# Kernel optimization log

Hardware: AMD Instinct MI355X
Metric: run time of the kernel (lower is better)

The kernel has to match this reference:

```python
import jax, jax.numpy as jnp
import numpy as np

TAU = 2.0        # leak time constant
CLAMP = 1000.0   # state clamp in LeakyRNN.recurrence
EPS = 1e-4       # eps in PolicyRNN.evaluate

B, T, H, NI, NA = 64, 2048, 256, 4, 2


def setup_inputs() -> dict:
    key = jax.random.key(0)
    ks = jax.random.split(key, 10)
    state = jax.random.normal(ks[0], (B, T, NI), jnp.float32)
    last_action = jax.random.normal(ks[1], (B, T, NA), jnp.float32)
    reward = jax.random.randint(ks[2], (B, T, NA), 0, 2).astype(jnp.float32)
    hidden_in = jnp.zeros((B, H), jnp.float32)
    W1 = jax.random.normal(ks[3], (H, NI + 2 * NA), jnp.float32) * np.float32(np.sqrt(2.0 / (NI + 2 * NA)))
    b1 = jnp.zeros((H,), jnp.float32)
    Wih = jax.random.normal(ks[4], (H, H), jnp.float32) * np.float32(np.sqrt(2.0 / H))
    Whh_raw = jax.random.normal(ks[5], (H, H), jnp.float32) * np.float32(0.5 / np.sqrt(H))
    W2 = jax.random.normal(ks[6], (H, H), jnp.float32) * np.float32(np.sqrt(2.0 / H))
    b2 = jnp.zeros((H,), jnp.float32)
    W3 = jax.random.normal(ks[7], (NA, H), jnp.float32) * np.float32(np.sqrt(2.0 / H))
    b3 = jnp.zeros((NA,), jnp.float32)
    Qs = jax.random.normal(ks[8], (B, T, NA), jnp.float32)
    # MultLayerAdaptiveSimple with alphas=[1,0]: weight1=[1,0], weight2=[0,1]
    mix_w = jnp.array([[1.0, 0.0], [0.0, 1.0]], jnp.float32)
    return dict(state=state, last_action=last_action, reward=reward,
                hidden_in=hidden_in, W1=W1, b1=b1, Wih=Wih, Whh_raw=Whh_raw,
                W2=W2, b2=b2, W3=W3, b3=b3, Qs=Qs, mix_w=mix_w)


def reference(state, last_action, reward, hidden_in, W1, b1, Wih, Whh_raw,
              W2, b2, W3, b3, Qs, mix_w):
    # (B,T,.) -> (T,B,.) time-major, matching permute(1,0,2)
    x = jnp.concatenate([reward, state, last_action], -1).transpose(1, 0, 2)
    x = jax.nn.relu(x @ W1.T + b1)                     # linear1 + relu

    # IdentityDiagonal parametrization: zero diagonal, subtract I/tau
    Whh = Whh_raw - jnp.diag(jnp.diag(Whh_raw)) - jnp.eye(H, dtype=Whh_raw.dtype) / TAU
    u = x @ Wih.T                                      # precompute input drive (T,B,H)
    leak = 1.0 - 1.0 / TAU

    def step(h, ut):
        h_new = jnp.clip(leak * h + ut + jax.nn.relu(h) @ Whh.T, -CLAMP, CLAMP)
        return h_new, h_new

    hidden_out, ys = jax.lax.scan(step, hidden_in, u)  # ys: (T,B,H)

    y = jax.nn.relu(ys @ W2.T + b2) @ W3.T + b3        # linear2+relu, linear3
    probs = y.transpose(1, 0, 2)                       # (B,T,NA)

    # evaluate() deterministic path with reward-indexed adaptive mixing
    z = (probs == 0.0).astype(probs.dtype) * EPS
    logp = jnp.log(jax.nn.softmax(probs, -1) + z)
    logq = jnp.log(jax.nn.softmax(Qs, -1) + z)
    # SumOne parametrization (p=1) on each MultLayer 2-vector
    w = jnp.clip(mix_w, -1.0, 1.0)
    table = w / jnp.sum(jnp.abs(w), axis=1, keepdims=True)   # (2,2)
    sel = table[reward[:, :, 0].astype(jnp.int32)]           # (B,T,2)
    mixed = logp * sel[..., :1] + logq * sel[..., 1:2]
    return jnp.exp(mixed), hidden_out
```

## Files before the change

kernel.cpp:

```cpp
#include <hip/hip_runtime.h>
#include <hip/hip_bf16.h>
#include <math.h>

#define Bn 64
#define Tn 2048
#define Hn 256

constexpr float LEAK    = 0.5f;
constexpr float NEGDIAG = -0.5f;
constexpr float CLAMP_V = 1000.0f;
constexpr float EPS_V   = 1e-4f;

typedef __attribute__((ext_vector_type(8))) short  short8;
typedef __attribute__((ext_vector_type(4))) float  f32x4;
typedef __attribute__((ext_vector_type(2))) float  f32x2;

#define FAST_BARRIER() do {                                   \
    asm volatile("s_waitcnt lgkmcnt(0)" ::: "memory");        \
    __builtin_amdgcn_s_barrier();                             \
    asm volatile("" ::: "memory");                            \
  } while (0)

__device__ inline short bf16_rne(float x) {
  __hip_bfloat16 h = __float2bfloat16(x);
  return *reinterpret_cast<short*>(&h);
}
__device__ inline float bf16_to_f(short s) {
  union { unsigned u; float f; } c; c.u = ((unsigned)(unsigned short)s) << 16;
  return c.f;
}
__device__ inline unsigned pack2(short a, short b) {
  return (unsigned)(unsigned short)a | ((unsigned)(unsigned short)b << 16);
}
__device__ inline void pkfma(f32x2& a, f32x2 x, f32x2 y) {
  asm("v_pk_fma_f32 %0, %1, %2, %0" : "+v"(a) : "v"(x), "v"(y));
}
#define SWZ(x, imm) __int_as_float(__builtin_amdgcn_ds_swizzle(__float_as_int(x), (imm)))

template <int CTRL>
__device__ __forceinline__ float dpp_recv(float x) {
  return __int_as_float(
      __builtin_amdgcn_update_dpp(0, __float_as_int(x), CTRL, 0xF, 0xF, true));
}

#define SA 40

__global__ __launch_bounds__(512) void g_u(
    const float* __restrict__ reward, const float* __restrict__ state,
    const float* __restrict__ last_action, const float* __restrict__ W1,
    const float* __restrict__ b1, const float* __restrict__ Wih,
    float* __restrict__ u)
{
  __shared__ short Ah[128*SA], Al[128*SA], Bh[256*SA], Bl[256*SA];
  __shared__ __align__(16) float inp_s[128][8];
  __shared__ __align__(16) float w1_s[256][8];
  __shared__ float b1_s[256];
  const int tid = threadIdx.x;
  const int r0  = blockIdx.x * 128;

  for (int idx = tid; idx < 2048; idx += 512) ((float*)w1_s)[idx] = W1[idx];
  if (tid < 256) b1_s[tid] = b1[tid];
  for (int idx = tid; idx < 1024; idx += 512) {
    int rr = idx >> 3, i = idx & 7;
    int r = r0 + rr, b = r & 63, t = r >> 6;
    long base = (long)b * Tn + t;
    float v;
    if (i < 2)      v = reward[base * 2 + i];
    else if (i < 6) v = state[base * 4 + (i - 2)];
    else            v = last_action[base * 2 + (i - 6)];
    inp_s[rr][i] = v;
  }

  const int w    = tid >> 6, lane = tid & 63;
  const int wm   = w >> 2, wn = w & 3;
  const int fr   = lane & 15, fk = lane >> 4;
  f32x4 acc[4][4];
  #pragma unroll
  for (int a = 0; a < 4; ++a)
    #pragma unroll
    for (int c = 0; c < 4; ++c) acc[a][c] = (f32x4){0.f, 0.f, 0.f, 0.f};

  __syncthreads();

  for (int ks = 0; ks < 8; ++ks) {
    const int k0 = ks * 32;
    if (ks) __syncthreads();
    for (int p = tid; p < 2048; p += 512) {
      int rr = p >> 4, kp = (p & 15) * 2;
      int k = k0 + kp;
      float4 iv0 = *reinterpret_cast<const float4*>(&inp_s[rr][0]);
      float4 iv1 = *reinterpret_cast<const float4*>(&inp_s[rr][4]);
      float4 wa0 = *reinterpret_cast<const float4*>(&w1_s[k][0]);
      float4 wa1 = *reinterpret_cast<const float4*>(&w1_s[k][4]);
      float4 wb0 = *reinterpret_cast<const float4*>(&w1_s[k+1][0]);
      float4 wb1 = *reinterpret_cast<const float4*>(&w1_s[k+1][4]);
      float s0 = b1_s[k], s1 = b1_s[k+1];
      s0 = fmaf(iv0.x, wa0.x, s0); s0 = fmaf(iv0.y, wa0.y, s0);
      s0 = fmaf(iv0.z, wa0.z, s0); s0 = fmaf(iv0.w, wa0.w, s0);
      s0 = fmaf(iv1.x, wa1.x, s0); s0 = fmaf(iv1.y, wa1.y, s0);
      s0 = fmaf(iv1.z, wa1.z, s0); s0 = fmaf(iv1.w, wa1.w, s0);
      s1 = fmaf(iv0.x, wb0.x, s1); s1 = fmaf(iv0.y, wb0.y, s1);
      s1 = fmaf(iv0.z, wb0.z, s1); s1 = fmaf(iv0.w, wb0.w, s1);
      s1 = fmaf(iv1.x, wb1.x, s1); s1 = fmaf(iv1.y, wb1.y, s1);
      s1 = fmaf(iv1.z, wb1.z, s1); s1 = fmaf(iv1.w, wb1.w, s1);
      float v0 = fmaxf(s0, 0.f), v1 = fmaxf(s1, 0.f);
      short h0 = bf16_rne(v0), h1 = bf16_rne(v1);
      short l0 = bf16_rne(v0 - bf16_to_f(h0)), l1 = bf16_rne(v1 - bf16_to_f(h1));
      int off = rr * SA + kp;
      *reinterpret_cast<unsigned*>(&Ah[off]) = pack2(h0, h1);
      *reinterpret_cast<unsigned*>(&Al[off]) = pack2(l0, l1);
    }
    for (int c = tid; c < 2048; c += 512) {
      int n = c >> 3, kc = (c & 7) * 4;
      float4 f = *reinterpret_cast<const float4*>(&Wih[n * 256 + k0 + kc]);
      short h0 = bf16_rne(f.x), h1 = bf16_rne(f.y), h2 = bf16_rne(f.z), h3 = bf16_rne(f.w);
      short l0 = bf16_rne(f.x - bf16_to_f(h0)), l1 = bf16_rne(f.y - bf16_to_f(h1));
      short l2 = bf16_rne(f.z - bf16_to_f(h2)), l3 = bf16_rne(f.w - bf16_to_f(h3));
      int off = n * SA + kc;
      *reinterpret_cast<uint2*>(&Bh[off]) = make_uint2(pack2(h0, h1), pack2(h2, h3));
      *reinterpret_cast<uint2*>(&Bl[off]) = make_uint2(pack2(l0, l1), pack2(l2, l3));
    }
    __syncthreads();
    short8 bhf[4], blf[4];
    #pragma unroll
    for (int nf = 0; nf < 4; ++nf) {
      const int brow = wn * 64 + nf * 16 + fr;
      bhf[nf] = *reinterpret_cast<const short8*>(&Bh[brow * SA + fk * 8]);
      blf[nf] = *reinterpret_cast<const short8*>(&Bl[brow * SA + fk * 8]);
    }
    #pragma unroll
    for (int mf = 0; mf < 4; ++mf) {
      const int arow = wm * 64 + mf * 16 + fr;
      short8 ah = *reinterpret_cast<const short8*>(&Ah[arow * SA + fk * 8]);
      short8 al = *reinterpret_cast<const short8*>(&Al[arow * SA + fk * 8]);
      #pragma unroll
      for (int nf = 0; nf < 4; ++nf) {
        acc[mf][nf] = __builtin_amdgcn_mfma_f32_16x16x32_bf16(ah, bhf[nf], acc[mf][nf], 0, 0, 0);
        acc[mf][nf] = __builtin_amdgcn_mfma_f32_16x16x32_bf16(ah, blf[nf], acc[mf][nf], 0, 0, 0);
        acc[mf][nf] = __builtin_amdgcn_mfma_f32_16x16x32_bf16(al, bhf[nf], acc[mf][nf], 0, 0, 0);
      }
    }
  }
  #pragma unroll
  for (int mf = 0; mf < 4; ++mf) {
    const int rbase = r0 + wm * 64 + mf * 16 + (lane >> 4) * 4;
    #pragma unroll
    for (int nf = 0; nf < 4; ++nf) {
      const int n = wn * 64 + nf * 16 + fr;
      #pragma unroll
      for (int j = 0; j < 4; ++j)
        u[(long)(rbase + j) * Hn + n] = acc[mf][nf][j];
    }
  }
}

__global__ __launch_bounds__(512, 2) void k_scan(
    const float* __restrict__ Whh_raw, const float* __restrict__ hidden_in,
    float* __restrict__ ubuf, float* __restrict__ out)
{
  __shared__ __align__(16) float rh[2][256];
  const int tid = threadIdx.x;
  const int w = tid >> 6;
  const int l = tid & 63;
  const int g = (l & 3) | ((l >> 1) & 0x1C);
  const int o = (l >> 2) & 1;
  const int b = blockIdx.x;
  const int key = ((g & 1) << 3) | ((g & 2) << 1) | ((g & 4) >> 1) | ((g & 8) >> 3);

  f32x2 w2[16][4];
  {
    const volatile float* Wv = Whh_raw;
    #pragma unroll
    for (int s = 0; s < 16; ++s) {
      const int j = (w << 5) + (o << 4) + (s ^ key);
      #pragma unroll
      for (int i = 0; i < 4; ++i) {
        const int k = (g << 3) + 2 * i;
        float a = Wv[j * 256 + k];
        float c = Wv[j * 256 + k + 1];
        if (k == j)     a = NEGDIAG;
        if (k + 1 == j) c = NEGDIAG;
        w2[s][i] = (f32x2){a, c};
      }
    }
  }

  const bool owner = (l < 32);
  const int j_own = (w << 5) + (o << 4) + key;

  const int row  = g >> 2;
  const int srot = (((g & 3) << 3) + (row << 2)) & 31;
  const int rd1  = row * 32 + srot;
  const int rd2  = row * 32 + ((srot + 4) & 31);
  const int wrow = j_own >> 5;
  const int wr   = wrow * 32 + (((j_own & 31) + (wrow << 2)) & 31);

  float h = 0.f, u_c = 0.f, u_n = 0.f;
  if (owner) {
    h   = hidden_in[b * Hn + j_own];
    u_c = ubuf[(long)b * Hn + j_own];
    u_n = ubuf[((long)Bn + b) * Hn + j_own];
  }
  const float* u_ptr  = ubuf + ((long)2 * Bn + b) * Hn + j_own;
  float*       ys_ptr = ubuf + (long)b * Hn + j_own;

#define SCAN_STEP(P)                                                         \
  {                                                                          \
    if (owner) rh[P][wr] = fmaxf(h, 0.f);                                    \
    FAST_BARRIER();                                                          \
    float u_pf = 0.f;                                                        \
    if (owner && t + 2 < Tn) u_pf = *u_ptr;                                  \
    const float4 ra = *reinterpret_cast<const float4*>(&rh[P][rd1]);         \
    const float4 rb = *reinterpret_cast<const float4*>(&rh[P][rd2]);         \
    const f32x2 rp0 = {ra.x, ra.y}, rp1 = {ra.z, ra.w};                      \
    const f32x2 rp2 = {rb.x, rb.y}, rp3 = {rb.z, rb.w};                      \
    float v[16];                                                             \
    _Pragma("unroll")                                                        \
    for (int s = 0; s < 16; ++s) {                                           \
      f32x2 c = {0.f, 0.f};                                                  \
      pkfma(c, rp0, w2[s][0]); pkfma(c, rp1, w2[s][1]);                      \
      pkfma(c, rp2, w2[s][2]); pkfma(c, rp3, w2[s][3]);                      \
      v[s] = c.x + c.y;                                                      \
    }                                                                        \
    _Pragma("unroll")                                                        \
    for (int s = 0; s < 8; ++s) v[s] += dpp_recv<0xB1>(v[s + 8]);            \
    _Pragma("unroll")                                                        \
    for (int s = 0; s < 4; ++s) v[s] += dpp_recv<0x4E>(v[s + 4]);            \
    _Pragma("unroll")                                                        \
    for (int s = 0; s < 2; ++s) v[s] += dpp_recv<0x128>(v[s + 2]);           \
    v[0] += SWZ(v[1], 0x401F);                                               \
    {                                                                        \
      float pa = v[0], pb = v[0];                                            \
      asm("v_permlane32_swap_b32 %0, %1" : "+v"(pa), "+v"(pb));              \
      v[0] = pa + pb;                                                        \
    }                                                                        \
    if (owner) {                                                             \
      float hn = fmaf(LEAK, h, u_c) + v[0];                                  \
      hn = fminf(fmaxf(hn, -CLAMP_V), CLAMP_V);                              \
      *ys_ptr = hn;                                                          \
      h = hn; u_c = u_n; u_n = u_pf;                                         \
    }                                                                        \
    ys_ptr += Bn * Hn;                                                       \
    u_ptr  += Bn * Hn;                                                       \
  }

  for (int tt = 0; tt < Tn; tt += 2) {
    { const int t = tt;     SCAN_STEP(0) }
    { const int t = tt + 1; SCAN_STEP(1) }
  }
#undef SCAN_STEP

  if (owner) out[(long)Bn * Tn * 2 + b * Hn + j_own] = h;
}

__global__ __launch_bounds__(512) void g_out(
    const float* __restrict__ ys, const float* __restrict__ W2,
    const float* __restrict__ b2, const float* __restrict__ W3,
    float* __restrict__ yout)
{
  __shared__ short Ah[128*SA], Al[128*SA], Bh[256*SA], Bl[256*SA];
  __shared__ float b2_s[256];
  __shared__ float w3_s[512];
  const int tid = threadIdx.x;
  const int r0  = blockIdx.x * 128;

  if (tid < 256) b2_s[tid] = b2[tid];
  if (tid < 512) w3_s[tid] = W3[tid];

  const int w    = tid >> 6, lane = tid & 63;
  const int wm   = w >> 2, wn = w & 3;
  const int fr   = lane & 15, fk = lane >> 4;
  f32x4 acc[4][4];
  #pragma unroll
  for (int a = 0; a < 4; ++a)
    #pragma unroll
    for (int c = 0; c < 4; ++c) acc[a][c] = (f32x4){0.f, 0.f, 0.f, 0.f};

  __syncthreads();

  for (int ks = 0; ks < 8; ++ks) {
    const int k0 = ks * 32;
    if (ks) __syncthreads();
    for (int c = tid; c < 1024; c += 512) {
      int rr = c >> 3, kc = (c & 7) * 4;
      float4 f = *reinterpret_cast<const float4*>(&ys[(long)(r0 + rr) * Hn + k0 + kc]);
      short h0 = bf16_rne(f.x), h1 = bf16_rne(f.y), h2 = bf16_rne(f.z), h3 = bf16_rne(f.w);
      short l0 = bf16_rne(f.x - bf16_to_f(h0)), l1 = bf16_rne(f.y - bf16_to_f(h1));
      short l2 = bf16_rne(f.z - bf16_to_f(h2)), l3 = bf16_rne(f.w - bf16_to_f(h3));
      int off = rr * SA + kc;
      *reinterpret_cast<uint2*>(&Ah[off]) = make_uint2(pack2(h0, h1), pack2(h2, h3));
      *reinterpret_cast<uint2*>(&Al[off]) = make_uint2(pack2(l0, l1), pack2(l2, l3));
    }
    for (int c = tid; c < 2048; c += 512) {
      int n = c >> 3, kc = (c & 7) * 4;
      float4 f = *reinterpret_cast<const float4*>(&W2[n * 256 + k0 + kc]);
      short h0 = bf16_rne(f.x), h1 = bf16_rne(f.y), h2 = bf16_rne(f.z), h3 = bf16_rne(f.w);
      short l0 = bf16_rne(f.x - bf16_to_f(h0)), l1 = bf16_rne(f.y - bf16_to_f(h1));
      short l2 = bf16_rne(f.z - bf16_to_f(h2)), l3 = bf16_rne(f.w - bf16_to_f(h3));
      int off = n * SA + kc;
      *reinterpret_cast<uint2*>(&Bh[off]) = make_uint2(pack2(h0, h1), pack2(h2, h3));
      *reinterpret_cast<uint2*>(&Bl[off]) = make_uint2(pack2(l0, l1), pack2(l2, l3));
    }
    __syncthreads();
    short8 bhf[4], blf[4];
    #pragma unroll
    for (int nf = 0; nf < 4; ++nf) {
      const int brow = wn * 64 + nf * 16 + fr;
      bhf[nf] = *reinterpret_cast<const short8*>(&Bh[brow * SA + fk * 8]);
      blf[nf] = *reinterpret_cast<const short8*>(&Bl[brow * SA + fk * 8]);
    }
    #pragma unroll
    for (int mf = 0; mf < 4; ++mf) {
      const int arow = wm * 64 + mf * 16 + fr;
      short8 ah = *reinterpret_cast<const short8*>(&Ah[arow * SA + fk * 8]);
      short8 al = *reinterpret_cast<const short8*>(&Al[arow * SA + fk * 8]);
      #pragma unroll
      for (int nf = 0; nf < 4; ++nf) {
        acc[mf][nf] = __builtin_amdgcn_mfma_f32_16x16x32_bf16(ah, bhf[nf], acc[mf][nf], 0, 0, 0);
        acc[mf][nf] = __builtin_amdgcn_mfma_f32_16x16x32_bf16(ah, blf[nf], acc[mf][nf], 0, 0, 0);
        acc[mf][nf] = __builtin_amdgcn_mfma_f32_16x16x32_bf16(al, bhf[nf], acc[mf][nf], 0, 0, 0);
      }
    }
  }

  float yp[4][4][2];
  #pragma unroll
  for (int mf = 0; mf < 4; ++mf)
    #pragma unroll
    for (int j = 0; j < 4; ++j) { yp[mf][j][0] = 0.f; yp[mf][j][1] = 0.f; }

  #pragma unroll
  for (int mf = 0; mf < 4; ++mf)
    #pragma unroll
    for (int nf = 0; nf < 4; ++nf) {
      const int n = wn * 64 + nf * 16 + fr;
      const float b2v = b2_s[n];
      const float w30 = w3_s[n], w31 = w3_s[256 + n];
      #pragma unroll
      for (int j = 0; j < 4; ++j) {
        float v = fmaxf(acc[mf][nf][j] + b2v, 0.f);
        yp[mf][j][0] = fmaf(v, w30, yp[mf][j][0]);
        yp[mf][j][1] = fmaf(v, w31, yp[mf][j][1]);
      }
    }
  #pragma unroll
  for (int off = 1; off < 16; off <<= 1) {
    #pragma unroll
    for (int mf = 0; mf < 4; ++mf)
      #pragma unroll
      for (int j = 0; j < 4; ++j) {
        yp[mf][j][0] += __shfl_xor(yp[mf][j][0], off);
        yp[mf][j][1] += __shfl_xor(yp[mf][j][1], off);
      }
  }

  __syncthreads();
  float* yred = reinterpret_cast<float*>(Ah);
  if (fr == 0) {
    #pragma unroll
    for (int mf = 0; mf < 4; ++mf)
      #pragma unroll
      for (int j = 0; j < 4; ++j) {
        int rl = wm * 64 + mf * 16 + (lane >> 4) * 4 + j;
        yred[(rl * 2 + 0) * 4 + wn] = yp[mf][j][0];
        yred[(rl * 2 + 1) * 4 + wn] = yp[mf][j][1];
      }
  }
  __syncthreads();
  if (tid < 256) {
    int rl = tid >> 1, a = tid & 1;
    const float* yr = &yred[(rl * 2 + a) * 4];
    float y = (yr[0] + yr[1]) + (yr[2] + yr[3]);
    int r = r0 + rl, b = r & 63, t = r >> 6;
    yout[((long)b * Tn + t) * 2 + a] = y;
  }
}

__global__ __launch_bounds__(256) void k_head(
    float* __restrict__ out, const float* __restrict__ Qs,
    const float* __restrict__ reward, const float* __restrict__ mix_w,
    const float* __restrict__ b3)
{
  const int idx = blockIdx.x * 256 + threadIdx.x;
  if (idx >= Bn * Tn) return;
  const long base = (long)idx * 2;
  float y0 = out[base]     + b3[0];
  float y1 = out[base + 1] + b3[1];
  float z0 = (y0 == 0.f) ? EPS_V : 0.f;
  float z1 = (y1 == 0.f) ? EPS_V : 0.f;

  float m  = fmaxf(y0, y1);
  float e0 = expf(y0 - m), e1 = expf(y1 - m), es = e0 + e1;
  float sp0 = e0 / es, sp1 = e1 / es;

  float q0 = Qs[base], q1 = Qs[base + 1];
  float mq = fmaxf(q0, q1);
  float f0 = expf(q0 - mq), f1 = expf(q1 - mq), fs = f0 + f1;
  float sq0 = f0 / fs, sq1 = f1 / fs;

  int ri = (int)reward[base];
  float m0 = fminf(fmaxf(mix_w[ri * 2 + 0], -1.f), 1.f);
  float m1 = fminf(fmaxf(mix_w[ri * 2 + 1], -1.f), 1.f);
  float den = fabsf(m0) + fabsf(m1);
  float s0 = m0 / den, s1 = m1 / den;

  out[base]     = expf(s0 * logf(sp0 + z0) + s1 * logf(sq0 + z0));
  out[base + 1] = expf(s0 * logf(sp1 + z1) + s1 * logf(sq1 + z1));
}

extern "C" void kernel_launch(void* const* d_in, const int* in_sizes, int n_in,
                              void* d_out, int out_size, void* d_ws, size_t ws_size,
                              hipStream_t stream)
{
  const float* state       = (const float*)d_in[0];
  const float* last_action = (const float*)d_in[1];
  const float* reward      = (const float*)d_in[2];
  const float* hidden_in   = (const float*)d_in[3];
  const float* W1          = (const float*)d_in[4];
  const float* b1          = (const float*)d_in[5];
  const float* Wih         = (const float*)d_in[6];
  const float* Whh_raw     = (const float*)d_in[7];
  const float* W2          = (const float*)d_in[8];
  const float* b2          = (const float*)d_in[9];
  const float* W3          = (const float*)d_in[10];
  const float* b3          = (const float*)d_in[11];
  const float* Qs          = (const float*)d_in[12];
  const float* mix_w       = (const float*)d_in[13];
  float* out = (float*)d_out;
  float* u   = (float*)d_ws;

  const int nrows = Tn * Bn;
  g_u   <<<nrows / 128, 512, 0, stream>>>(reward, state, last_action, W1, b1, Wih, u);
  k_scan<<<Bn,           512, 0, stream>>>(Whh_raw, hidden_in, u, out);
  g_out <<<nrows / 128, 512, 0, stream>>>(u, W2, b2, W3, out);
  k_head<<<nrows / 256, 256, 0, stream>>>(out, Qs, reward, mix_w, b3);
}
```

Measured before the change: 1.458 ms.

## Halve scan block to 256 threads with each lane owning one hidden unit

Restructures the recurrent scan so each block uses 4 waves of 256 threads, with every lane owning one output unit instead of only half the lanes owning units. Each lane now holds 16x8 packed weight pairs covering 16 K elements, which doubles the FMAs per lane but shortens the cross-lane reduction (no permlane32 swap, fewer DPP steps) and makes the per-step barrier cheaper with fewer waves. The cost is double the register use for weights and longer serial FMA chains per step, which sit on the latency-bound critical path of the sequential scan.

```diff
diff --git a/kernel.cpp b/kernel.cpp
--- a/kernel.cpp
+++ b/kernel.cpp
@@ -154,92 +154,89 @@
   }
 }
 
-__global__ __launch_bounds__(512, 2) void k_scan(
+__global__ __launch_bounds__(256, 1) void k_scan(
     const float* __restrict__ Whh_raw, const float* __restrict__ hidden_in,
     float* __restrict__ ubuf, float* __restrict__ out)
 {
   __shared__ __align__(16) float rh[2][256];
   const int tid = threadIdx.x;
-  const int w = tid >> 6;
-  const int l = tid & 63;
-  const int g = (l & 3) | ((l >> 1) & 0x1C);
-  const int o = (l >> 2) & 1;
-  const int b = blockIdx.x;
-  const int key = ((g & 1) << 3) | ((g & 2) << 1) | ((g & 4) >> 1) | ((g & 8) >> 3);
-
-  f32x2 w2[16][4];
+  const int w  = tid >> 6;
+  const int l  = tid & 63;
+  const int aa = l >> 4;
+  const int g  = l & 15;
+  const int b  = blockIdx.x;
+
+  f32x2 w2[16][8];
+  #pragma unroll
+  for (int s = 0; s < 16; ++s) {
+    const int j = (w << 6) + (aa << 4) + (s ^ g);
+    #pragma unroll
+    for (int i = 0; i < 8; ++i) {
+      const int k = (g << 4) + 2 * i;
+      float x0 = Whh_raw[j * 256 + k];
+      float x1 = Whh_raw[j * 256 + k + 1];
+      if (k == j)     x0 = NEGDIAG;
+      if (k + 1 == j) x1 = NEGDIAG;
+      w2[s][i] = (f32x2){x0, x1};
+    }
+  }
+
+  const int j_own = (w << 6) + (aa << 4) + g;
+
+  int rd[4];
   {
-    const volatile float* Wv = Whh_raw;
-    #pragma unroll
-    for (int s = 0; s < 16; ++s) {
-      const int j = (w << 5) + (o << 4) + (s ^ key);
-      #pragma unroll
-      for (int i = 0; i < 4; ++i) {
-        const int k = (g << 3) + 2 * i;
-        float a = Wv[j * 256 + k];
-        float c = Wv[j * 256 + k + 1];
-        if (k == j)     a = NEGDIAG;
-        if (k + 1 == j) c = NEGDIAG;
-        w2[s][i] = (f32x2){a, c};
-      }
-    }
-  }
-
-  const bool owner = (l < 32);
-  const int j_own = (w << 5) + (o << 4) + key;
-
-  const int row  = g >> 2;
-  const int srot = (((g & 3) << 3) + (row << 2)) & 31;
-  const int rd1  = row * 32 + srot;
-  const int rd2  = row * 32 + ((srot + 4) & 31);
-  const int wrow = j_own >> 5;
-  const int wr   = wrow * 32 + (((j_own & 31) + (wrow << 2)) & 31);
-
-  float h = 0.f, u_c = 0.f, u_n = 0.f;
-  if (owner) {
-    h   = hidden_in[b * Hn + j_own];
-    u_c = ubuf[(long)b * Hn + j_own];
-    u_n = ubuf[((long)Bn + b) * Hn + j_own];
-  }
+    const int r = g >> 1;
+    #pragma unroll
+    for (int q = 0; q < 4; ++q) {
+      const int lc = ((g & 1) << 4) + (q << 2);
+      rd[q] = (r << 5) + ((lc + (r << 2)) & 31);
+    }
+  }
+  const int wr_r = j_own >> 5;
+  const int wr   = (wr_r << 5) + (((j_own & 31) + (wr_r << 2)) & 31);
+
+  float h   = hidden_in[b * Hn + j_own];
+  float u_c = ubuf[(long)b * Hn + j_own];
+  float u_n = ubuf[((long)Bn + b) * Hn + j_own];
   const float* u_ptr  = ubuf + ((long)2 * Bn + b) * Hn + j_own;
   float*       ys_ptr = ubuf + (long)b * Hn + j_own;
 
 #define SCAN_STEP(P)                                                         \
   {                                                                          \
-    if (owner) rh[P][wr] = fmaxf(h, 0.f);                                    \
+    rh[P][wr] = fmaxf(h, 0.f);                                               \
     FAST_BARRIER();                                                          \
     float u_pf = 0.f;                                                        \
-    if (owner && t + 2 < Tn) u_pf = *u_ptr;                                  \
-    const float4 ra = *reinterpret_cast<const float4*>(&rh[P][rd1]);         \
-    const float4 rb = *reinterpret_cast<const float4*>(&rh[P][rd2]);         \
-    const f32x2 rp0 = {ra.x, ra.y}, rp1 = {ra.z, ra.w};                      \
-    const f32x2 rp2 = {rb.x, rb.y}, rp3 = {rb.z, rb.w};                      \
+    if (t + 2 < Tn) u_pf = *u_ptr;                                           \
+    const float4 r0q = *reinterpret_cast<const float4*>(&rh[P][rd[0]]);      \
+    const float4 r1q = *reinterpret_cast<const float4*>(&rh[P][rd[1]]);      \
+    const float4 r2q = *reinterpret_cast<const float4*>(&rh[P][rd[2]]);      \
+    const float4 r3q = *reinterpret_cast<const float4*>(&rh[P][rd[3]]);      \
+    const f32x2 rp0 = {r0q.x, r0q.y}, rp1 = {r0q.z, r0q.w};                  \
+    const f32x2 rp2 = {r1q.x, r1q.y}, rp3 = {r1q.z, r1q.w};                  \
+    const f32x2 rp4 = {r2q.x, r2q.y}, rp5 = {r2q.z, r2q.w};                  \
+    const f32x2 rp6 = {r3q.x, r3q.y}, rp7 = {r3q.z, r3q.w};                  \
     float v[16];                                                             \
     _Pragma("unroll")                                                        \
     for (int s = 0; s < 16; ++s) {                                           \
       f32x2 c = {0.f, 0.f};                                                  \
       pkfma(c, rp0, w2[s][0]); pkfma(c, rp1, w2[s][1]);                      \
       pkfma(c, rp2, w2[s][2]); pkfma(c, rp3, w2[s][3]);                      \
+      pkfma(c, rp4, w2[s][4]); pkfma(c, rp5, w2[s][5]);                      \
+      pkfma(c, rp6, w2[s][6]); pkfma(c, rp7, w2[s][7]);                      \
       v[s] = c.x + c.y;                                                      \
     }                                                                        \
+            \
     _Pragma("unroll")                                                        \
-    for (int s = 0; s < 8; ++s) v[s] += dpp_recv<0xB1>(v[s + 8]);            \
+    for (int s = 0; s < 8; ++s) v[s] += dpp_recv<0x128>(v[s + 8]);   \
     _Pragma("unroll")                                                        \
-    for (int s = 0; s < 4; ++s) v[s] += dpp_recv<0x4E>(v[s + 4]);            \
-    _Pragma("unroll")                                                        \
-    for (int s = 0; s < 2; ++s) v[s] += dpp_recv<0x128>(v[s + 2]);           \
-    v[0] += SWZ(v[1], 0x401F);                                               \
-    {                                                                        \
-      float pa = v[0], pb = v[0];                                            \
-      asm("v_permlane32_swap_b32 %0, %1" : "+v"(pa), "+v"(pb));              \
-      v[0] = pa + pb;                                                        \
-    }                                                                        \
-    if (owner) {                                                             \
-      float hn = fmaf(LEAK, h, u_c) + v[0];                                  \
-      hn = fminf(fmaxf(hn, -CLAMP_V), CLAMP_V);                              \
-      *ys_ptr = hn;                                                          \
-      h = hn; u_c = u_n; u_n = u_pf;                                         \
-    }                                                                        \
+    for (int s = 0; s < 4; ++s) v[s] += SWZ(v[s + 4], 0x101F);       \
+    v[0] += dpp_recv<0x4E>(v[2]);                                    \
+    v[1] += dpp_recv<0x4E>(v[3]);                                            \
+    v[0] += dpp_recv<0xB1>(v[1]);                                    \
+    float hn = fmaf(LEAK, h, u_c) + v[0];                                    \
+    hn = fminf(fmaxf(hn, -CLAMP_V), CLAMP_V);                                \
+    *ys_ptr = hn;                                                            \
+    h = hn; u_c = u_n; u_n = u_pf;                                           \
     ys_ptr += Bn * Hn;                                                       \
     u_ptr  += Bn * Hn;                                                       \
   }
@@ -250,7 +247,7 @@
   }
 #undef SCAN_STEP
 
-  if (owner) out[(long)Bn * Tn * 2 + b * Hn + j_own] = h;
+  out[(long)Bn * Tn * 2 + b * Hn + j_own] = h;
 }
 
 __global__ __launch_bounds__(512) void g_out(
@@ -431,7 +428,7 @@
 
   const int nrows = Tn * Bn;
   g_u   <<<nrows / 128, 512, 0, stream>>>(reward, state, last_action, W1, b1, Wih, u);
-  k_scan<<<Bn,           512, 0, stream>>>(Whh_raw, hidden_in, u, out);
+  k_scan<<<Bn,           256, 0, stream>>>(Whh_raw, hidden_in, u, out);
   g_out <<<nrows / 128, 512, 0, stream>>>(u, W2, b2, W3, out);
   k_head<<<nrows / 256, 256, 0, stream>>>(out, Qs, reward, mix_w, b3);
 }
```

Result: slower. 1.555 ms (+6.7%).
